# Performance work log

Hardware: AMD Instinct MI355X
Metric: run time of the kernel (lower is better)

The kernel has to match this reference:

```python
import jax
import jax.numpy as jnp
from jax import lax
import numpy as np

B, ND, H, W = 8, 8, 512, 512
CONF = 0.9
MARGIN = 3.0
MIN_CLUSTER = 50
MAX_X = 102.4
MPP0, MPP1 = 0.2, 0.2
K = 32  # max clusters (torch version grows an unbounded python list)


def setup_inputs() -> dict:
    key = jax.random.key(0)
    k1, k2, k3, k4, k5, k6 = jax.random.split(key, 6)
    return {
        "seg": jax.random.uniform(k1, (B, 1, H, W), dtype=jnp.float32),
        "embedding": jax.random.normal(k2, (B, ND, H, W), dtype=jnp.float32),
        "offset_pred": jax.random.normal(k3, (B, 1, H, W), dtype=jnp.float32),
        "z_pred": jax.random.normal(k4, (B, 1, H, W), dtype=jnp.float32),
        "intrinsic": jax.random.normal(k5, (B, 3, 3), dtype=jnp.float32),
        "extrinsic": jax.random.normal(k6, (B, 4, 4), dtype=jnp.float32),
    }


def _cluster_one(seg_flat, emb_flat):
    # seg_flat: [N], emb_flat: [N, ND]. Greedy sequential embedding clustering
    # (naive_cluster_nd): running-mean centers, assign to nearest center if
    # within MARGIN else open a new one. Fixed K slots; counts>0 marks active.
    nd = emb_flat.shape[1]

    def step(carry, xs):
        centers, counts = carry  # [K, nd], [K]
        s, e = xs
        valid = s >= CONF
        d = jnp.sqrt(jnp.sum((centers - e) ** 2, axis=1))
        d = jnp.where(counts > 0, d, jnp.inf)
        cid_min = jnp.argmin(d).astype(jnp.int32)
        join = d[cid_min] < MARGIN
        n_active = jnp.sum(counts > 0).astype(jnp.int32)
        cid = jnp.where(join, cid_min, jnp.minimum(n_active, K - 1))
        cnt = counts[cid]
        new_c = jnp.where(join, (centers[cid] * cnt + e) / (cnt + 1.0), e)
        centers = jnp.where(valid, centers.at[cid].set(new_c), centers)
        counts = jnp.where(valid, counts.at[cid].add(1.0), counts)
        return (centers, counts), jnp.where(valid, cid, -1)

    init = (jnp.zeros((K, nd), emb_flat.dtype), jnp.zeros((K,), emb_flat.dtype))
    (_, _), cids = lax.scan(step, init, (seg_flat, emb_flat))
    return cids  # [N] int32, -1 = background


def reference(seg, embedding, offset_pred, z_pred, intrinsic, extrinsic):
    b, nd, h, w = embedding.shape
    seg_flat = seg[:, 0].reshape(b, h * w)
    emb_flat = embedding.reshape(b, nd, h * w).transpose(0, 2, 1)  # [B, N, nd]
    cids = jax.vmap(_cluster_one)(seg_flat, emb_flat).reshape(b, h, w)
    lanes = jnp.where(cids >= 0, cids + 1, 0)  # [B, H, W], 0 = background

    # mean_col_by_row_with_offset_z: per (batch, lane, row) mean of col+offset and z
    offset_y = jax.nn.sigmoid(offset_pred[:, 0])          # [B, H, W]
    x_adj = jnp.arange(w, dtype=seg.dtype)[None, None, :] + offset_y
    zc = z_pred[:, 0]
    b_idx = jnp.arange(b)[:, None, None]
    h_idx = jnp.arange(h)[None, :, None]
    seg_ids = ((b_idx * (K + 1) + lanes) * h + h_idx).reshape(-1)
    num = b * (K + 1) * h

    def ssum(v):
        return jax.ops.segment_sum(v.reshape(-1), seg_ids, num_segments=num).reshape(b, K + 1, h)[:, 1:]

    cnt = ssum(jnp.ones((b, h, w), seg.dtype))            # [B, K, H]
    mean_x = ssum(x_adj) / jnp.maximum(cnt, 1.0)
    mean_z = ssum(zc) / jnp.maximum(cnt, 1.0)

    size = cnt.sum(-1)                                    # cluster pixel count
    n_rows = (cnt > 0).sum(-1)                            # rows per lane
    valid = (cnt > 0) & (size[:, :, None] >= MIN_CLUSTER) & (n_rows[:, :, None] >= 2)

    # ego-coordinate transform from forward()
    x_world = (MAX_X / MPP0 - (jnp.arange(h, dtype=seg.dtype) + 0.5)) * MPP0  # [H]
    x_world = jnp.broadcast_to(x_world, (b, K, h))
    y_world = -(mean_x - (w // 2)) * MPP1
    points = jnp.stack([x_world, y_world, mean_z], axis=1)  # [B, 3, K, H]
    points = jnp.where(valid[:, None], points, 0.0)
    return points, valid
```

## Files before the change

kernel.cpp:

```cpp
#include <hip/hip_runtime.h>

#define HW_ (512 * 512)
#define B_ 8
#define H_ 512
#define W_ 512
#define K_ 32
#define CH_ 16
#define CHPIX_ (HW_ / CH_)

typedef float float2v __attribute__((ext_vector_type(2)));

__global__ void k_count(const float* __restrict__ seg, int* __restrict__ chunkCnt) {
  const int blk = blockIdx.x;
  const int t = threadIdx.x;
  const float4* __restrict__ s4 = (const float4*)(seg + (size_t)blk * CHPIX_) + (size_t)t * 16;
  int cnt = 0;
#pragma unroll
  for (int j = 0; j < 16; ++j) {
    float4 v = s4[j];
    cnt += (v.x >= 0.9f) + (v.y >= 0.9f) + (v.z >= 0.9f) + (v.w >= 0.9f);
  }
  __shared__ int red[256];
  red[t] = cnt;
  __syncthreads();
  for (int off = 128; off > 0; off >>= 1) {
    if (t < off) red[t] += red[t + off];
    __syncthreads();
  }
  if (t == 0) chunkCnt[blk] = red[0];
}

__global__ void k_scan(const int* __restrict__ chunkCnt, int* __restrict__ chunkBase,
                       int* __restrict__ nvalid, int cap) {
  const int t = threadIdx.x;
  if (t < B_ * CH_) {
    const int b = t / CH_, c = t % CH_;
    int base = 0;
    for (int q = 0; q < c; ++q) base += chunkCnt[b * CH_ + q];
    chunkBase[t] = base;
    if (c == CH_ - 1) nvalid[b] = min(base + chunkCnt[t], cap);
  }
}

__global__ void k_fill(const float* __restrict__ seg, const float* __restrict__ emb,
                       const int* __restrict__ chunkBase, unsigned char* __restrict__ lanes,
                       int* __restrict__ idxC, float* __restrict__ embC, int cap) {
  const int blk = blockIdx.x;
  const int b = blk / CH_;
  const int t = threadIdx.x;
  const size_t pixbase = (size_t)blk * CHPIX_ + (size_t)t * 64;
  const float4* __restrict__ s4 = (const float4*)(seg + pixbase);

  int cnt = 0;
#pragma unroll
  for (int j = 0; j < 16; ++j) {
    float4 v = s4[j];
    cnt += (v.x >= 0.9f) + (v.y >= 0.9f) + (v.z >= 0.9f) + (v.w >= 0.9f);
  }
  __shared__ int pre[256];
  pre[t] = cnt;
  __syncthreads();
  for (int off = 1; off < 256; off <<= 1) {
    int mine = pre[t];
    int add = (t >= off) ? pre[t - off] : 0;
    __syncthreads();
    pre[t] = mine + add;
    __syncthreads();
  }
  int w = chunkBase[blk] + pre[t] - cnt;

  uint4 z = {0u, 0u, 0u, 0u};
  uint4* lz = (uint4*)(lanes + pixbase);
  lz[0] = z; lz[1] = z; lz[2] = z; lz[3] = z;

  const float* __restrict__ eb = emb + (size_t)b * 8 * HW_;
  const int pixInB = (int)(pixbase - (size_t)b * HW_);
  for (int j = 0; j < 16; ++j) {
    float4 v = s4[j];
    float sv[4] = {v.x, v.y, v.z, v.w};
#pragma unroll
    for (int q = 0; q < 4; ++q) {
      if (sv[q] >= 0.9f && w < cap) {
        const int p = pixInB + j * 4 + q;
        idxC[(size_t)b * cap + w] = p;
        float* dst = embC + ((size_t)b * cap + w) * 8;
#pragma unroll
        for (int dd = 0; dd < 8; ++dd) dst[dd] = eb[(size_t)dd * HW_ + p];
        ++w;
      }
    }
  }
}


#define TILE_ 32

__device__ __forceinline__ void stage16(const float* g, float* l) {
  __builtin_amdgcn_global_load_lds(
      (const __attribute__((address_space(1))) void*)g,
      (__attribute__((address_space(3))) void*)l, 16, 0, 0);
}

#define RLU(V, L) ((unsigned)__builtin_amdgcn_readlane((int)(V), (L)))
#define PKF(A, B, C) __builtin_elementwise_fma((A), (B), (C))

#define STEPQ(J, US, LS)                                                             \
  do {                                                                               \
    float2v t01 = C01 - e01_##US;                                                    \
    float2v t23 = C23 - e23_##US;                                                    \
    float2v t45 = C45 - e45_##US;                                                    \
    float2v t67 = C67 - e67_##US;                                                    \
    float2v p = t01 * t01;                                                           \
    p = PKF(t23, t23, p);                                                            \
    p = PKF(t45, t45, p);                                                            \
    p = PKF(t67, t67, p);                                                            \
    float dsq = p.x + p.y;                                                           \
    unsigned db = __float_as_uint(dsq);                                              \
    unsigned dbm = db > emptyBits ? db : emptyBits;         \
    unsigned mn = (dbm & 0xFFFFFFE0u) | (unsigned)cl;                                \
    unsigned mr;                                                                     \
    mr = (unsigned)__builtin_amdgcn_update_dpp(0, (int)mn, 0xB1, 0xF, 0xF, true);    \
    mn = mn < mr ? mn : mr;                                                          \
    mr = (unsigned)__builtin_amdgcn_update_dpp(0, (int)mn, 0x4E, 0xF, 0xF, true);    \
    mn = mn < mr ? mn : mr;                                                          \
    mr = (unsigned)__builtin_amdgcn_update_dpp(0, (int)mn, 0x141, 0xF, 0xF, true);   \
    mn = mn < mr ? mn : mr;                                                          \
    mr = (unsigned)__builtin_amdgcn_update_dpp(0, (int)mn, 0x140, 0xF, 0xF, true);   \
    mn = mn < mr ? mn : mr;                                                          \
    unsigned q0 = RLU(mn, 0), q1 = RLU(mn, 16);                                      \
    unsigned mv = q0 < q1 ? q0 : q1;                            \
    bool join = mv < 0x41100000u;            \
    int cid = join ? (int)(mv & 31u) : (nact < 31 ? nact : 31);                      \
    nact += join ? 0 : 1;                                                            \
    bool own = (cl == cid);                                                          \
    float wj = join ? inv : 1.0f;                                                    \
    float w = own ? wj : 0.0f;                                                       \
    float2v wv = {w, w};                                                             \
    C01 = PKF(t01, -wv, C01);                                          \
    C23 = PKF(t23, -wv, C23);                                                        \
    C45 = PKF(t45, -wv, C45);                                                        \
    C67 = PKF(t67, -wv, C67);                                                        \
    cnt += own ? 1.0f : 0.0f;                                                        \
    inv = __builtin_amdgcn_rcpf(cnt + 1.0f);          \
    emptyBits = own ? 0u : emptyBits;                                                \
    pk |= (unsigned long long)(unsigned)(cid + 1) << (((J) & 7) * 8);                \
    if (((J) & 7) == 7) {                                                            \
      if (lane == 0) *(unsigned long long*)(cptr + ((J) & ~7)) = pk;                 \
      pk = 0ULL;                                                                     \
    }                                                                                \
    if ((J) < TILE_ - 2) {       \
      e01_##LS = ebq[((J) + 2) * 4 + 0];                                             \
      e23_##LS = ebq[((J) + 2) * 4 + 1];                                             \
      e45_##LS = ebq[((J) + 2) * 4 + 2];                                             \
      e67_##LS = ebq[((J) + 2) * 4 + 3];                                             \
    }                                                                                \
  } while (0)

__global__ __launch_bounds__(64, 1) void k_cluster(const float* __restrict__ embC,
                                                   const int* __restrict__ nvalid,
                                                   unsigned char* __restrict__ cidArr,
                                                   int cap) {
  __shared__ float lds[512];
  const int b = blockIdx.x;
  const int lane = threadIdx.x;
  const int cl = lane & 31;
  const int n = nvalid[b];
  if (n <= 0) return;
  const int nTiles = (n + TILE_ - 1) / TILE_;

  const float* src = embC + (size_t)b * cap * 8 + lane * 4;
  unsigned char* cidB = cidArr + (size_t)b * HW_;

  float2v C01 = {0.f, 0.f}, C23 = C01, C45 = C01, C67 = C01;
  float2v e01_0, e23_0, e45_0, e67_0;
  float2v e01_1, e23_1, e45_1, e67_1;
  float2v e01_2, e23_2, e45_2, e67_2;
  float cnt = 0.f, inv = 1.0f;
  unsigned emptyBits = 0x7F800000u;
  int nact = 0;
  unsigned long long pk = 0ULL;

  stage16(src, lds);
  asm volatile("s_waitcnt vmcnt(0)" ::: "memory");
  __builtin_amdgcn_sched_barrier(0);

  for (int ti = 0; ti < nTiles; ++ti) {
    const bool more = (ti + 1 < nTiles);
    const float2v* ebq = (const float2v*)((const char*)lds + (ti & 1) * 1024);
    unsigned char* cptr = cidB + ti * TILE_;

    e01_0 = ebq[0]; e23_0 = ebq[1]; e45_0 = ebq[2]; e67_0 = ebq[3];
    e01_1 = ebq[4]; e23_1 = ebq[5]; e45_1 = ebq[6]; e67_1 = ebq[7];

    if (more)
      stage16(src + (size_t)(ti + 1) * 256, lds + ((ti + 1) & 1) * 256);

    STEPQ(0, 0, 2);  STEPQ(1, 1, 0);  STEPQ(2, 2, 1);  STEPQ(3, 0, 2);
    STEPQ(4, 1, 0);  STEPQ(5, 2, 1);  STEPQ(6, 0, 2);  STEPQ(7, 1, 0);
    STEPQ(8, 2, 1);  STEPQ(9, 0, 2);  STEPQ(10, 1, 0); STEPQ(11, 2, 1);
    STEPQ(12, 0, 2); STEPQ(13, 1, 0); STEPQ(14, 2, 1); STEPQ(15, 0, 2);
    STEPQ(16, 1, 0); STEPQ(17, 2, 1); STEPQ(18, 0, 2); STEPQ(19, 1, 0);
    STEPQ(20, 2, 1); STEPQ(21, 0, 2); STEPQ(22, 1, 0); STEPQ(23, 2, 1);
    STEPQ(24, 0, 2); STEPQ(25, 1, 0); STEPQ(26, 2, 1); STEPQ(27, 0, 2);
    STEPQ(28, 1, 0); STEPQ(29, 2, 1); STEPQ(30, 0, 2); STEPQ(31, 1, 0);

    if (more) {
      asm volatile("s_waitcnt vmcnt(4)" ::: "memory");
      __builtin_amdgcn_sched_barrier(0);
    }
  }
}

__global__ void k_scatter(const unsigned char* __restrict__ cidArr,
                          const int* __restrict__ idxC, const int* __restrict__ nvalid,
                          unsigned char* __restrict__ lanes, int cap) {
  const int b = blockIdx.y;
  const int n = nvalid[b];
  for (int j = blockIdx.x * blockDim.x + threadIdx.x; j < n; j += gridDim.x * blockDim.x) {
    lanes[(size_t)b * HW_ + idxC[(size_t)b * cap + j]] = cidArr[(size_t)b * HW_ + j];
  }
}

__global__ void k_rowsum(const unsigned char* __restrict__ lanes,
                         const float* __restrict__ offp, const float* __restrict__ zp,
                         float* __restrict__ cnt, float* __restrict__ sx,
                         float* __restrict__ sz) {
  const int bh = blockIdx.x;
  const int b = bh >> 9, h = bh & 511;
  __shared__ float sc[33], sxx[33], szz[33];
  const int t = threadIdx.x;
  if (t < 33) { sc[t] = 0.f; sxx[t] = 0.f; szz[t] = 0.f; }
  __syncthreads();
  const size_t base = (size_t)bh * W_;
  for (int x = t; x < W_; x += 256) {
    int ln = lanes[base + x];
    float o = offp[base + x];
    float sig = 1.0f / (1.0f + expf(-o));
    float xa = (float)x + sig;
    float zv = zp[base + x];
    atomicAdd(&sc[ln], 1.0f);
    atomicAdd(&sxx[ln], xa);
    atomicAdd(&szz[ln], zv);
  }
  __syncthreads();
  if (t >= 1 && t < 33) {
    size_t o = ((size_t)b * K_ + (t - 1)) * H_ + h;
    cnt[o] = sc[t]; sx[o] = sxx[t]; sz[o] = szz[t];
  }
}

__global__ void k_final(const float* __restrict__ cnt, const float* __restrict__ sx,
                        const float* __restrict__ sz, float* __restrict__ out) {
  const int bk = blockIdx.x;
  const int b = bk >> 5, k = bk & 31;
  const int h = threadIdx.x;
  const size_t o = (size_t)bk * H_ + h;
  float c = cnt[o];
  float sc_ = c, sn = (c > 0.f) ? 1.f : 0.f;
#pragma unroll
  for (int off = 32; off >= 1; off >>= 1) {
    sc_ += __shfl_down(sc_, off);
    sn += __shfl_down(sn, off);
  }
  __shared__ float rs[8], rn[8], tot[2];
  const int wid = h >> 6, lid = h & 63;
  if (lid == 0) { rs[wid] = sc_; rn[wid] = sn; }
  __syncthreads();
  if (h == 0) {
    float a = 0, bb = 0;
#pragma unroll
    for (int q = 0; q < 8; ++q) { a += rs[q]; bb += rn[q]; }
    tot[0] = a; tot[1] = bb;
  }
  __syncthreads();
  float size = tot[0], nrows = tot[1];
  bool valid = (c > 0.f) && (size >= 50.f) && (nrows >= 2.f);
  float mx = sx[o] / fmaxf(c, 1.f);
  float mz = sz[o] / fmaxf(c, 1.f);
  float xw = (512.0f - ((float)h + 0.5f)) * 0.2f;
  float yw = -(mx - 256.0f) * 0.2f;
  out[((size_t)(b * 3 + 0) * K_ + k) * H_ + h] = valid ? xw : 0.f;
  out[((size_t)(b * 3 + 1) * K_ + k) * H_ + h] = valid ? yw : 0.f;
  out[((size_t)(b * 3 + 2) * K_ + k) * H_ + h] = valid ? mz : 0.f;
  out[(size_t)B_ * 3 * K_ * H_ + (size_t)bk * H_ + h] = valid ? 1.f : 0.f;
}

extern "C" void kernel_launch(void* const* d_in, const int* in_sizes, int n_in,
                              void* d_out, int out_size, void* d_ws, size_t ws_size,
                              hipStream_t stream) {
  const float* seg  = (const float*)d_in[0];
  const float* emb  = (const float*)d_in[1];
  const float* offp = (const float*)d_in[2];
  const float* zp   = (const float*)d_in[3];
  float* out = (float*)d_out;
  char* ws = (char*)d_ws;

  const size_t lanesOff = 0;
  const size_t cntOff   = (size_t)B_ * HW_;
  const size_t sxOff    = cntOff + (size_t)B_ * K_ * H_ * 4;
  const size_t szOff    = sxOff  + (size_t)B_ * K_ * H_ * 4;
  const size_t nvOff    = szOff  + (size_t)B_ * K_ * H_ * 4;
  const size_t ccOff    = nvOff + 256;
  const size_t cbOff    = ccOff + 1024;
  const size_t cidOff   = cbOff + 1024;
  const size_t idxOff   = cidOff + (size_t)B_ * HW_;
  size_t avail = (ws_size > idxOff + 8192) ? (ws_size - idxOff - 8192) : 0;
  long long capLL = (long long)(avail / ((size_t)B_ * 36));
  if (capLL > (long long)HW_) capLL = HW_;
  if (capLL < 2) capLL = 2;
  capLL &= ~1LL;
  const int cap = (int)capLL;
  const size_t embOff = idxOff + (size_t)B_ * cap * 4;

  unsigned char* lanes = (unsigned char*)(ws + lanesOff);
  float* cnt = (float*)(ws + cntOff);
  float* sx  = (float*)(ws + sxOff);
  float* sz  = (float*)(ws + szOff);
  int* nvalid = (int*)(ws + nvOff);
  int* chunkCnt  = (int*)(ws + ccOff);
  int* chunkBase = (int*)(ws + cbOff);
  unsigned char* cidArr = (unsigned char*)(ws + cidOff);
  int* idxC   = (int*)(ws + idxOff);
  float* embC = (float*)(ws + embOff);

  k_count<<<B_ * CH_, 256, 0, stream>>>(seg, chunkCnt);
  k_scan<<<1, 128, 0, stream>>>(chunkCnt, chunkBase, nvalid, cap);
  k_fill<<<B_ * CH_, 256, 0, stream>>>(seg, emb, chunkBase, lanes, idxC, embC, cap);
  k_cluster<<<B_, 64, 0, stream>>>(embC, nvalid, cidArr, cap);
  k_scatter<<<dim3(64, B_), 256, 0, stream>>>(cidArr, idxC, nvalid, lanes, cap);
  k_rowsum<<<B_ * H_, 256, 0, stream>>>(lanes, offp, zp, cnt, sx, sz);
  k_final<<<B_ * K_, H_, 0, stream>>>(cnt, sx, sz, out);
}
```

Before: 3.035 ms.

## Speculatively precompute next-step distance to shorten greedy clustering critical path

Rewrites the sequential clustering step so that the distance from each center to the next embedding is computed speculatively, assuming no update. The pending update is then folded in with a scalar correction, dsq = w^2*d + w*(-2g) + d_spec. This takes the packed center update and distance reduction off the loop-carried dependency chain. It also deepens the LDS prefetch from a 3-slot to a 4-slot ring that pre-loads the next tile's first entries across the tile boundary. The price is extra per-step vector math and registers, and the changed rounding could flip near-tie or margin decisions.

Result: slower. 3.252 ms (+7.2%).

```diff
diff --git a/kernel.cpp b/kernel.cpp
--- a/kernel.cpp
+++ b/kernel.cpp
@@ -104,17 +104,16 @@
 #define RLU(V, L) ((unsigned)__builtin_amdgcn_readlane((int)(V), (L)))
 #define PKF(A, B, C) __builtin_elementwise_fma((A), (B), (C))
 
-#define STEPQ(J, US, LS)                                                             \
+#define LOADSLOT4(LS, EBQ, LIDX)          \
+  e01_##LS = (EBQ)[(LIDX) * 4 + 0];       \
+  e23_##LS = (EBQ)[(LIDX) * 4 + 1];       \
+  e45_##LS = (EBQ)[(LIDX) * 4 + 2];       \
+  e67_##LS = (EBQ)[(LIDX) * 4 + 3];
+
+#define STEPC(J, US)                                                                 \
   do {                                                                               \
-    float2v t01 = C01 - e01_##US;                                                    \
-    float2v t23 = C23 - e23_##US;                                                    \
-    float2v t45 = C45 - e45_##US;                                                    \
-    float2v t67 = C67 - e67_##US;                                                    \
-    float2v p = t01 * t01;                                                           \
-    p = PKF(t23, t23, p);                                                            \
-    p = PKF(t45, t45, p);                                                            \
-    p = PKF(t67, t67, p);                                                            \
-    float dsq = p.x + p.y;                                                           \
+                                            \
+    float dsq = __builtin_fmaf(wp, __builtin_fmaf(wp, dsqq, m2g), dspec);            \
     unsigned db = __float_as_uint(dsq);                                              \
     unsigned dbm = db > emptyBits ? db : emptyBits;         \
     unsigned mn = (dbm & 0xFFFFFFE0u) | (unsigned)cl;                                \
@@ -133,26 +132,34 @@
     int cid = join ? (int)(mv & 31u) : (nact < 31 ? nact : 31);                      \
     nact += join ? 0 : 1;                                                            \
     bool own = (cl == cid);                                                          \
-    float wj = join ? inv : 1.0f;                                                    \
-    float w = own ? wj : 0.0f;                                                       \
-    float2v wv = {w, w};                                                             \
-    C01 = PKF(t01, -wv, C01);                                          \
-    C23 = PKF(t23, -wv, C23);                                                        \
-    C45 = PKF(t45, -wv, C45);                                                        \
-    C67 = PKF(t67, -wv, C67);                                                        \
+    float w = own ? (join ? inv : 1.0f) : 0.0f;                                      \
+        \
+    float2v wp2 = {wp, wp};                                                          \
+    C01 = PKF(wp2, t01, C01); C23 = PKF(wp2, t23, C23);                              \
+    C45 = PKF(wp2, t45, C45); C67 = PKF(wp2, t67, C67);                              \
+    t01 = PKF(-wp2, t01, s01); t23 = PKF(-wp2, t23, s23);                            \
+    t45 = PKF(-wp2, t45, s45); t67 = PKF(-wp2, t67, s67);                            \
+    s01 = e01_##US - C01; s23 = e23_##US - C23;                                      \
+    s45 = e45_##US - C45; s67 = e67_##US - C67;                                      \
+    float2v p = s01 * s01;                                                           \
+    p = PKF(s23, s23, p);                                                            \
+    p = PKF(s45, s45, p);                                                            \
+    p = PKF(s67, s67, p);                                                            \
+    dspec = p.x + p.y;                                                               \
+    float2v gv = t01 * s01;                                                          \
+    gv = PKF(t23, s23, gv);                                                          \
+    gv = PKF(t45, s45, gv);                                                          \
+    gv = PKF(t67, s67, gv);                                                          \
+    m2g = -2.0f * (gv.x + gv.y);                                                     \
+    dsqq = dsq;                                                                      \
+    wp = w;                                                                          \
     cnt += own ? 1.0f : 0.0f;                                                        \
-    inv = __builtin_amdgcn_rcpf(cnt + 1.0f);          \
+    inv = __builtin_amdgcn_rcpf(cnt + 1.0f);                     \
     emptyBits = own ? 0u : emptyBits;                                                \
     pk |= (unsigned long long)(unsigned)(cid + 1) << (((J) & 7) * 8);                \
     if (((J) & 7) == 7) {                                                            \
       if (lane == 0) *(unsigned long long*)(cptr + ((J) & ~7)) = pk;                 \
       pk = 0ULL;                                                                     \
-    }                                                                                \
-    if ((J) < TILE_ - 2) {       \
-      e01_##LS = ebq[((J) + 2) * 4 + 0];                                             \
-      e23_##LS = ebq[((J) + 2) * 4 + 1];                                             \
-      e45_##LS = ebq[((J) + 2) * 4 + 2];                                             \
-      e67_##LS = ebq[((J) + 2) * 4 + 3];                                             \
     }                                                                                \
   } while (0)
 
@@ -172,10 +179,13 @@
   unsigned char* cidB = cidArr + (size_t)b * HW_;
 
   float2v C01 = {0.f, 0.f}, C23 = C01, C45 = C01, C67 = C01;
+  float2v t01 = C01, t23 = C01, t45 = C01, t67 = C01;
+  float2v s01, s23, s45, s67;
   float2v e01_0, e23_0, e45_0, e67_0;
   float2v e01_1, e23_1, e45_1, e67_1;
   float2v e01_2, e23_2, e45_2, e67_2;
-  float cnt = 0.f, inv = 1.0f;
+  float2v e01_3, e23_3, e45_3, e67_3;
+  float cnt = 0.f, inv = 1.0f, wp = 0.f, m2g = 0.f, dsqq = 0.f, dspec;
   unsigned emptyBits = 0x7F800000u;
   int nact = 0;
   unsigned long long pk = 0ULL;
@@ -183,31 +193,65 @@
   stage16(src, lds);
   asm volatile("s_waitcnt vmcnt(0)" ::: "memory");
   __builtin_amdgcn_sched_barrier(0);
+  {
+    const float2v* eb0 = (const float2v*)lds;
+    s01 = eb0[0]; s23 = eb0[1]; s45 = eb0[2]; s67 = eb0[3];
+    float2v p = s01 * s01;
+    p = PKF(s23, s23, p);
+    p = PKF(s45, s45, p);
+    p = PKF(s67, s67, p);
+    dspec = p.x + p.y;
+    LOADSLOT4(0, eb0, 1)
+    LOADSLOT4(1, eb0, 2)
+    LOADSLOT4(2, eb0, 3)
+  }
 
   for (int ti = 0; ti < nTiles; ++ti) {
     const bool more = (ti + 1 < nTiles);
     const float2v* ebq = (const float2v*)((const char*)lds + (ti & 1) * 1024);
+    const float2v* ebqN = (const float2v*)((const char*)lds + ((ti + 1) & 1) * 1024);
     unsigned char* cptr = cidB + ti * TILE_;
-
-    e01_0 = ebq[0]; e23_0 = ebq[1]; e45_0 = ebq[2]; e67_0 = ebq[3];
-    e01_1 = ebq[4]; e23_1 = ebq[5]; e45_1 = ebq[6]; e67_1 = ebq[7];
 
     if (more)
       stage16(src + (size_t)(ti + 1) * 256, lds + ((ti + 1) & 1) * 256);
 
-    STEPQ(0, 0, 2);  STEPQ(1, 1, 0);  STEPQ(2, 2, 1);  STEPQ(3, 0, 2);
-    STEPQ(4, 1, 0);  STEPQ(5, 2, 1);  STEPQ(6, 0, 2);  STEPQ(7, 1, 0);
-    STEPQ(8, 2, 1);  STEPQ(9, 0, 2);  STEPQ(10, 1, 0); STEPQ(11, 2, 1);
-    STEPQ(12, 0, 2); STEPQ(13, 1, 0); STEPQ(14, 2, 1); STEPQ(15, 0, 2);
-    STEPQ(16, 1, 0); STEPQ(17, 2, 1); STEPQ(18, 0, 2); STEPQ(19, 1, 0);
-    STEPQ(20, 2, 1); STEPQ(21, 0, 2); STEPQ(22, 1, 0); STEPQ(23, 2, 1);
-    STEPQ(24, 0, 2); STEPQ(25, 1, 0); STEPQ(26, 2, 1); STEPQ(27, 0, 2);
-    STEPQ(28, 1, 0); STEPQ(29, 2, 1); STEPQ(30, 0, 2); STEPQ(31, 1, 0);
+    STEPC(0, 0);  LOADSLOT4(3, ebq, 4)
+    STEPC(1, 1);  LOADSLOT4(0, ebq, 5)
+    STEPC(2, 2);  LOADSLOT4(1, ebq, 6)
+    STEPC(3, 3);  LOADSLOT4(2, ebq, 7)
+    STEPC(4, 0);  LOADSLOT4(3, ebq, 8)
+    STEPC(5, 1);  LOADSLOT4(0, ebq, 9)
+    STEPC(6, 2);  LOADSLOT4(1, ebq, 10)
+    STEPC(7, 3);  LOADSLOT4(2, ebq, 11)
+    STEPC(8, 0);  LOADSLOT4(3, ebq, 12)
+    STEPC(9, 1);  LOADSLOT4(0, ebq, 13)
+    STEPC(10, 2); LOADSLOT4(1, ebq, 14)
+    STEPC(11, 3); LOADSLOT4(2, ebq, 15)
+    STEPC(12, 0); LOADSLOT4(3, ebq, 16)
+    STEPC(13, 1); LOADSLOT4(0, ebq, 17)
+    STEPC(14, 2); LOADSLOT4(1, ebq, 18)
+    STEPC(15, 3); LOADSLOT4(2, ebq, 19)
+    STEPC(16, 0); LOADSLOT4(3, ebq, 20)
+    STEPC(17, 1); LOADSLOT4(0, ebq, 21)
+    STEPC(18, 2); LOADSLOT4(1, ebq, 22)
+    STEPC(19, 3); LOADSLOT4(2, ebq, 23)
+    STEPC(20, 0); LOADSLOT4(3, ebq, 24)
+    STEPC(21, 1); LOADSLOT4(0, ebq, 25)
+    STEPC(22, 2); LOADSLOT4(1, ebq, 26)
+    STEPC(23, 3); LOADSLOT4(2, ebq, 27)
+    STEPC(24, 0); LOADSLOT4(3, ebq, 28)
+    STEPC(25, 1); LOADSLOT4(0, ebq, 29)
+    STEPC(26, 2); LOADSLOT4(1, ebq, 30)
+    STEPC(27, 3); LOADSLOT4(2, ebq, 31)
 
     if (more) {
-      asm volatile("s_waitcnt vmcnt(4)" ::: "memory");
+      asm volatile("s_waitcnt vmcnt(3)" ::: "memory");
       __builtin_amdgcn_sched_barrier(0);
     }
+    STEPC(28, 0); if (more) { LOADSLOT4(3, ebqN, 0) }
+    STEPC(29, 1); if (more) { LOADSLOT4(0, ebqN, 1) }
+    STEPC(30, 2); if (more) { LOADSLOT4(1, ebqN, 2) }
+    STEPC(31, 3); if (more) { LOADSLOT4(2, ebqN, 3) }
   }
 }
 
```

## Shorten serial cluster-step critical path with DPP row broadcast and permlane32 swap

Applied to the files above, without the earlier changes.

Rewrites the per-pixel step of the sequential clustering loop so that the cross-row min reduction stays in vector registers, using a DPP row broadcast and a permlane32 swap (ds_bpermute as fallback), instead of two readlanes. The weight for the own-lane center update is computed per lane from the reduced key. A precomputed new-cluster weight is carried over from the previous step, which keeps the scalar cid/nact bookkeeping off the dependency chain. The distance sum is also split into two independent FMA chains. This aims to cut latency in the strictly serial loop, but adds more lane-crossing ops and depends on exact DPP/permlane semantics for correctness.

Result: slower. 3.309 ms (+9.0%).

```diff
diff --git a/kernel.cpp b/kernel.cpp
--- a/kernel.cpp
+++ b/kernel.cpp
@@ -95,6 +95,12 @@
 
 #define TILE_ 32
 
+#if defined(__has_builtin)
+#if __has_builtin(__builtin_amdgcn_permlane32_swap)
+#define HAVE_PLSWAP 1
+#endif
+#endif
+
 __device__ __forceinline__ void stage16(const float* g, float* l) {
   __builtin_amdgcn_global_load_lds(
       (const __attribute__((address_space(1))) void*)g,
@@ -110,15 +116,16 @@
     float2v t23 = C23 - e23_##US;                                                    \
     float2v t45 = C45 - e45_##US;                                                    \
     float2v t67 = C67 - e67_##US;                                                    \
-    float2v p = t01 * t01;                                                           \
-    p = PKF(t23, t23, p);                                                            \
-    p = PKF(t45, t45, p);                                                            \
-    p = PKF(t67, t67, p);                                                            \
-    float dsq = p.x + p.y;                                                           \
+    float2v pA = t01 * t01;                                                          \
+    pA = PKF(t23, t23, pA);                                                          \
+    float2v pB = t45 * t45;                                                          \
+    pB = PKF(t67, t67, pB);                                                          \
+    pA = pA + pB;                                                                    \
+    float dsq = pA.x + pA.y;                                                         \
     unsigned db = __float_as_uint(dsq);                                              \
     unsigned dbm = db > emptyBits ? db : emptyBits;         \
-    unsigned mn = (dbm & 0xFFFFFFE0u) | (unsigned)cl;                                \
-    unsigned mr;                                                                     \
+    unsigned key = (dbm & 0xFFFFFFE0u) | (unsigned)cl;                               \
+    unsigned mn = key, mr;                                                           \
     mr = (unsigned)__builtin_amdgcn_update_dpp(0, (int)mn, 0xB1, 0xF, 0xF, true);    \
     mn = mn < mr ? mn : mr;                                                          \
     mr = (unsigned)__builtin_amdgcn_update_dpp(0, (int)mn, 0x4E, 0xF, 0xF, true);    \
@@ -127,34 +134,63 @@
     mn = mn < mr ? mn : mr;                                                          \
     mr = (unsigned)__builtin_amdgcn_update_dpp(0, (int)mn, 0x140, 0xF, 0xF, true);   \
     mn = mn < mr ? mn : mr;                                                          \
-    unsigned q0 = RLU(mn, 0), q1 = RLU(mn, 16);                                      \
-    unsigned mv = q0 < q1 ? q0 : q1;                            \
-    bool join = mv < 0x41100000u;            \
-    int cid = join ? (int)(mv & 31u) : (nact < 31 ? nact : 31);                      \
-    nact += join ? 0 : 1;                                                            \
-    bool own = (cl == cid);                                                          \
-    float wj = join ? inv : 1.0f;                                                    \
-    float w = own ? wj : 0.0f;                                                       \
-    float2v wv = {w, w};                                                             \
-    C01 = PKF(t01, -wv, C01);                                          \
-    C23 = PKF(t23, -wv, C23);                                                        \
-    C45 = PKF(t45, -wv, C45);                                                        \
-    C67 = PKF(t67, -wv, C67);                                                        \
-    cnt += own ? 1.0f : 0.0f;                                                        \
-    inv = __builtin_amdgcn_rcpf(cnt + 1.0f);          \
-    emptyBits = own ? 0u : emptyBits;                                                \
+                  \
+    mr = (unsigned)__builtin_amdgcn_update_dpp((int)mn, (int)mn, 0x142, 0xE, 0xF,    \
+                                               false);                               \
+    mn = mn < mr ? mn : mr;                 \
+                                              \
+    float wJoin = (key == mn) ? inv : 0.0f;                                          \
+    bool join_v = mn < 0x41100000u;          \
+    float w_pre = join_v ? wJoin : wNew;                                             \
+    float w;                                                                         \
+    WSWAP(w, w_pre)                                                                  \
+    float2v w2 = {w, w};                                                             \
+    C01 = PKF(t01, -w2, C01);                                          \
+    C23 = PKF(t23, -w2, C23);                                                        \
+    C45 = PKF(t45, -w2, C45);                                                        \
+    C67 = PKF(t67, -w2, C67);                                                        \
+    bool ownb = w > 0.0f;                                                            \
+    cnt = ownb ? cntp1 : cnt;                                                        \
+    cntp1 = cnt + 1.0f;                                                              \
+    inv = __builtin_amdgcn_rcpf(cntp1);                                              \
+    emptyBits = ownb ? 0u : emptyBits;                                               \
+                              \
+    unsigned s_mv = RLU(mn, 16);                                                     \
+    bool join_s = s_mv < 0x41100000u;                                                \
+    int nactc = nact < 31 ? nact : 31;                                               \
+    int cid = join_s ? (int)(s_mv & 31u) : nactc;                                    \
+    nact += join_s ? 0 : 1;                                                          \
+    int nactc2 = nact < 31 ? nact : 31;                                              \
+    wNew = ((unsigned)cl == (unsigned)nactc2) ? 1.0f : 0.0f;                         \
     pk |= (unsigned long long)(unsigned)(cid + 1) << (((J) & 7) * 8);                \
     if (((J) & 7) == 7) {                                                            \
       if (lane == 0) *(unsigned long long*)(cptr + ((J) & ~7)) = pk;                 \
       pk = 0ULL;                                                                     \
     }                                                                                \
-    if ((J) < TILE_ - 2) {       \
+    if ((J) < TILE_ - 2) {             \
       e01_##LS = ebq[((J) + 2) * 4 + 0];                                             \
       e23_##LS = ebq[((J) + 2) * 4 + 1];                                             \
       e45_##LS = ebq[((J) + 2) * 4 + 2];                                             \
       e67_##LS = ebq[((J) + 2) * 4 + 3];                                             \
     }                                                                                \
   } while (0)
+
+#if HAVE_PLSWAP
+#define WSWAP(W, WPRE)                                                           \
+  {                                                                              \
+    auto ws_ = __builtin_amdgcn_permlane32_swap(__float_as_uint(WPRE),           \
+                                                __float_as_uint(WPRE), false,    \
+                                                false);                          \
+    float wls_ = selA ? __uint_as_float(ws_[0]) : __uint_as_float(ws_[1]);       \
+    W = (lane < 32) ? wls_ : (WPRE);                                             \
+  }
+#else
+#define WSWAP(W, WPRE)                                                           \
+  {                                                                              \
+    int wb_ = __builtin_amdgcn_ds_bpermute(bpa, (int)__float_as_uint(WPRE));     \
+    W = __uint_as_float((unsigned)wb_);                                          \
+  }
+#endif
 
 __global__ __launch_bounds__(64, 1) void k_cluster(const float* __restrict__ embC,
                                                    const int* __restrict__ nvalid,
@@ -171,11 +207,23 @@
   const float* src = embC + (size_t)b * cap * 8 + lane * 4;
   unsigned char* cidB = cidArr + (size_t)b * HW_;
 
+#if HAVE_PLSWAP
+  bool selA;
+  {
+    unsigned lv = (unsigned)lane;
+    auto pr = __builtin_amdgcn_permlane32_swap(lv, lv, false, false);
+    selA = (RLU(pr[0], 0) == 32u);
+  }
+#else
+  const int bpa = ((lane < 32) ? (lane + 32) : lane) * 4;
+#endif
+
   float2v C01 = {0.f, 0.f}, C23 = C01, C45 = C01, C67 = C01;
   float2v e01_0, e23_0, e45_0, e67_0;
   float2v e01_1, e23_1, e45_1, e67_1;
   float2v e01_2, e23_2, e45_2, e67_2;
-  float cnt = 0.f, inv = 1.0f;
+  float cnt = 0.f, cntp1 = 1.0f, inv = 1.0f;
+  float wNew = (cl == 0) ? 1.0f : 0.0f;
   unsigned emptyBits = 0x7F800000u;
   int nact = 0;
   unsigned long long pk = 0ULL;
```

## Pack two batch clustering scans into one wave using both 32-lane halves

Applied to the files above, without the earlier changes.

The sequential clustering kernel now processes two batch images per 64-lane wavefront. Each half-wave holds one image's 32 cluster centers, and both half-minimums are read out per step, so four waves run instead of eight. Because the per-step DPP reductions already stay within each 32-lane half, the lanes that previously duplicated work now do useful work, and the grid is halved. The distance sum is also split into two shorter FMA chains to cut dependency latency. The cost is extra scalar bookkeeping per step, plus padding the shorter image up to the longer image's tile count, which could lengthen the serial critical path.

After: 4.155 ms. 1.37x slower.

```diff
diff --git a/kernel.cpp b/kernel.cpp
--- a/kernel.cpp
+++ b/kernel.cpp
@@ -104,20 +104,30 @@
 #define RLU(V, L) ((unsigned)__builtin_amdgcn_readlane((int)(V), (L)))
 #define PKF(A, B, C) __builtin_elementwise_fma((A), (B), (C))
 
+#define OFFP(P) ((P) * 32 + (((P) >= 16) ? 512 : 0))
+
+#define LOADSLOT4(LS, EB, P)                                    \
+  e01_##LS = *(const float2v*)((EB) + OFFP(P));                 \
+  e23_##LS = *(const float2v*)((EB) + OFFP(P) + 8);             \
+  e45_##LS = *(const float2v*)((EB) + OFFP(P) + 16);            \
+  e67_##LS = *(const float2v*)((EB) + OFFP(P) + 24);
+
 #define STEPQ(J, US, LS)                                                             \
   do {                                                                               \
     float2v t01 = C01 - e01_##US;                                                    \
     float2v t23 = C23 - e23_##US;                                                    \
     float2v t45 = C45 - e45_##US;                                                    \
     float2v t67 = C67 - e67_##US;                                                    \
-    float2v p = t01 * t01;                                                           \
-    p = PKF(t23, t23, p);                                                            \
-    p = PKF(t45, t45, p);                                                            \
-    p = PKF(t67, t67, p);                                                            \
-    float dsq = p.x + p.y;                                                           \
+    float2v pA = t01 * t01;                                                          \
+    pA = PKF(t23, t23, pA);                                                          \
+    float2v pB = t45 * t45;                                                          \
+    pB = PKF(t67, t67, pB);                                                          \
+    pA = pA + pB;                                                                    \
+    float dsq = pA.x + pA.y;                                                         \
     unsigned db = __float_as_uint(dsq);                                              \
     unsigned dbm = db > emptyBits ? db : emptyBits;         \
     unsigned mn = (dbm & 0xFFFFFFE0u) | (unsigned)cl;                                \
+    unsigned key = mn;                                                               \
     unsigned mr;                                                                     \
     mr = (unsigned)__builtin_amdgcn_update_dpp(0, (int)mn, 0xB1, 0xF, 0xF, true);    \
     mn = mn < mr ? mn : mr;                                                          \
@@ -127,32 +137,43 @@
     mn = mn < mr ? mn : mr;                                                          \
     mr = (unsigned)__builtin_amdgcn_update_dpp(0, (int)mn, 0x140, 0xF, 0xF, true);   \
     mn = mn < mr ? mn : mr;                                                          \
+    (void)key;                                                                       \
     unsigned q0 = RLU(mn, 0), q1 = RLU(mn, 16);                                      \
-    unsigned mv = q0 < q1 ? q0 : q1;                            \
-    bool join = mv < 0x41100000u;            \
-    int cid = join ? (int)(mv & 31u) : (nact < 31 ? nact : 31);                      \
-    nact += join ? 0 : 1;                                                            \
-    bool own = (cl == cid);                                                          \
-    float wj = join ? inv : 1.0f;                                                    \
+    unsigned q2 = RLU(mn, 32), q3 = RLU(mn, 48);                                     \
+    unsigned mvA = q0 < q1 ? q0 : q1;                           \
+    unsigned mvB = q2 < q3 ? q2 : q3;                                                \
+    bool joinA = mvA < 0x41100000u;          \
+    bool joinB = mvB < 0x41100000u;                                                  \
+    int cidA = joinA ? (int)(mvA & 31u) : (nactA < 31 ? nactA : 31);                 \
+    int cidB = joinB ? (int)(mvB & 31u) : (nactB < 31 ? nactB : 31);                 \
+    nactA += joinA ? 0 : 1;                                                          \
+    nactB += joinB ? 0 : 1;                                                          \
+    int vcid = hi ? cidB : cidA;                                  \
+    bool own = (cl == vcid);                                                         \
+    float jsA = joinA ? 1.0f : 0.0f;                               \
+    float jsB = joinB ? 1.0f : 0.0f;                                                 \
+    float vjs = hi ? jsB : jsA;                                   \
+    float wj = (vjs != 0.0f) ? inv : 1.0f;                                           \
     float w = own ? wj : 0.0f;                                                       \
-    float2v wv = {w, w};                                                             \
-    C01 = PKF(t01, -wv, C01);                                          \
-    C23 = PKF(t23, -wv, C23);                                                        \
-    C45 = PKF(t45, -wv, C45);                                                        \
-    C67 = PKF(t67, -wv, C67);                                                        \
-    cnt += own ? 1.0f : 0.0f;                                                        \
-    inv = __builtin_amdgcn_rcpf(cnt + 1.0f);          \
+    float2v w2 = {w, w};                                                             \
+    C01 = PKF(t01, -w2, C01);                                          \
+    C23 = PKF(t23, -w2, C23);                                                        \
+    C45 = PKF(t45, -w2, C45);                                                        \
+    C67 = PKF(t67, -w2, C67);                                                        \
+    cnt = own ? cntp1 : cnt;                                                         \
+    cntp1 = cnt + 1.0f;                                                              \
+    inv = __builtin_amdgcn_rcpf(cntp1);               \
     emptyBits = own ? 0u : emptyBits;                                                \
-    pk |= (unsigned long long)(unsigned)(cid + 1) << (((J) & 7) * 8);                \
+    pkA |= (unsigned long long)(unsigned)(cidA + 1) << (((J) & 7) * 8);              \
+    pkB |= (unsigned long long)(unsigned)(cidB + 1) << (((J) & 7) * 8);              \
     if (((J) & 7) == 7) {                                                            \
-      if (lane == 0) *(unsigned long long*)(cptr + ((J) & ~7)) = pk;                 \
-      pk = 0ULL;                                                                     \
+      if (lane == 0) *(unsigned long long*)(cpA + ((J) & ~7)) = pkA;                 \
+      if (lane == 32) *(unsigned long long*)(cpB + ((J) & ~7)) = pkB;                \
+      pkA = 0ULL;                                                                    \
+      pkB = 0ULL;                                                                    \
     }                                                                                \
-    if ((J) < TILE_ - 2) {       \
-      e01_##LS = ebq[((J) + 2) * 4 + 0];                                             \
-      e23_##LS = ebq[((J) + 2) * 4 + 1];                                             \
-      e45_##LS = ebq[((J) + 2) * 4 + 2];                                             \
-      e67_##LS = ebq[((J) + 2) * 4 + 3];                                             \
+    if ((J) < TILE_ - 2) {            \
+      LOADSLOT4(LS, ebase, (J) + 2)                                                  \
     }                                                                                \
   } while (0)
 
@@ -160,40 +181,48 @@
                                                    const int* __restrict__ nvalid,
                                                    unsigned char* __restrict__ cidArr,
                                                    int cap) {
-  __shared__ float lds[512];
-  const int b = blockIdx.x;
+  __shared__ float lds[1024];
+  const int blk = blockIdx.x;
   const int lane = threadIdx.x;
+  const bool hi = lane >= 32;
   const int cl = lane & 31;
-  const int n = nvalid[b];
-  if (n <= 0) return;
-  const int nTiles = (n + TILE_ - 1) / TILE_;
-
-  const float* src = embC + (size_t)b * cap * 8 + lane * 4;
-  unsigned char* cidB = cidArr + (size_t)b * HW_;
+  const int bA = 2 * blk, bB = 2 * blk + 1;
+  const int nA = nvalid[bA], nB = nvalid[bB];
+  const int nMax = nA > nB ? nA : nB;
+  if (nMax <= 0) return;
+  const int nTiles = (nMax + TILE_ - 1) / TILE_;
+
+  const float* srcv = embC + (size_t)(hi ? bB : bA) * cap * 8 + (size_t)cl * 4;
+  unsigned char* cA = cidArr + (size_t)bA * HW_;
+  unsigned char* cB = cidArr + (size_t)bB * HW_;
 
   float2v C01 = {0.f, 0.f}, C23 = C01, C45 = C01, C67 = C01;
   float2v e01_0, e23_0, e45_0, e67_0;
   float2v e01_1, e23_1, e45_1, e67_1;
   float2v e01_2, e23_2, e45_2, e67_2;
-  float cnt = 0.f, inv = 1.0f;
+  float cnt = 0.f, cntp1 = 1.0f, inv = 1.0f;
   unsigned emptyBits = 0x7F800000u;
-  int nact = 0;
-  unsigned long long pk = 0ULL;
-
-  stage16(src, lds);
+  int nactA = 0, nactB = 0;
+  unsigned long long pkA = 0ULL, pkB = 0ULL;
+
+  stage16(srcv, lds);
+  stage16(srcv + 128, lds + 256);
   asm volatile("s_waitcnt vmcnt(0)" ::: "memory");
   __builtin_amdgcn_sched_barrier(0);
 
   for (int ti = 0; ti < nTiles; ++ti) {
     const bool more = (ti + 1 < nTiles);
-    const float2v* ebq = (const float2v*)((const char*)lds + (ti & 1) * 1024);
-    unsigned char* cptr = cidB + ti * TILE_;
-
-    e01_0 = ebq[0]; e23_0 = ebq[1]; e45_0 = ebq[2]; e67_0 = ebq[3];
-    e01_1 = ebq[4]; e23_1 = ebq[5]; e45_1 = ebq[6]; e67_1 = ebq[7];
-
-    if (more)
-      stage16(src + (size_t)(ti + 1) * 256, lds + ((ti + 1) & 1) * 256);
+    const char* ebase = (const char*)lds + (ti & 1) * 2048 + (hi ? 512 : 0);
+    unsigned char* cpA = cA + ti * TILE_;
+    unsigned char* cpB = cB + ti * TILE_;
+
+    LOADSLOT4(0, ebase, 0)
+    LOADSLOT4(1, ebase, 1)
+
+    if (more) {
+      stage16(srcv + (size_t)(ti + 1) * 256, lds + ((ti + 1) & 1) * 512);
+      stage16(srcv + (size_t)(ti + 1) * 256 + 128, lds + ((ti + 1) & 1) * 512 + 256);
+    }
 
     STEPQ(0, 0, 2);  STEPQ(1, 1, 0);  STEPQ(2, 2, 1);  STEPQ(3, 0, 2);
     STEPQ(4, 1, 0);  STEPQ(5, 2, 1);  STEPQ(6, 0, 2);  STEPQ(7, 1, 0);
@@ -205,7 +234,7 @@
     STEPQ(28, 1, 0); STEPQ(29, 2, 1); STEPQ(30, 0, 2); STEPQ(31, 1, 0);
 
     if (more) {
-      asm volatile("s_waitcnt vmcnt(4)" ::: "memory");
+      asm volatile("s_waitcnt vmcnt(8)" ::: "memory");
       __builtin_amdgcn_sched_barrier(0);
     }
   }
@@ -304,7 +333,7 @@
   const size_t cbOff    = ccOff + 1024;
   const size_t cidOff   = cbOff + 1024;
   const size_t idxOff   = cidOff + (size_t)B_ * HW_;
-  size_t avail = (ws_size > idxOff + 8192) ? (ws_size - idxOff - 8192) : 0;
+  size_t avail = (ws_size > idxOff + 16384) ? (ws_size - idxOff - 16384) : 0;
   long long capLL = (long long)(avail / ((size_t)B_ * 36));
   if (capLL > (long long)HW_) capLL = HW_;
   if (capLL < 2) capLL = 2;
@@ -326,7 +355,7 @@
   k_count<<<B_ * CH_, 256, 0, stream>>>(seg, chunkCnt);
   k_scan<<<1, 128, 0, stream>>>(chunkCnt, chunkBase, nvalid, cap);
   k_fill<<<B_ * CH_, 256, 0, stream>>>(seg, emb, chunkBase, lanes, idxC, embC, cap);
-  k_cluster<<<B_, 64, 0, stream>>>(embC, nvalid, cidArr, cap);
+  k_cluster<<<B_ / 2, 64, 0, stream>>>(embC, nvalid, cidArr, cap);
   k_scatter<<<dim3(64, B_), 256, 0, stream>>>(cidArr, idxC, nvalid, lanes, cap);
   k_rowsum<<<B_ * H_, 256, 0, stream>>>(lanes, offp, zp, cnt, sx, sz);
   k_final<<<B_ * K_, H_, 0, stream>>>(cnt, sx, sz, out);
```
